# Optimization experiments

Hardware: AMD Instinct MI355X
Metric: run time of the kernel (lower is better)

## Reference

```python
import jax, jax.numpy as jnp
import numpy as np

N = 50000      # nodes
E = 800000     # edges
F_IN = 128     # num_node_features
H = 128        # hidden_channels
C = 10         # num_classes
G = 512        # graphs in batch


def setup_inputs() -> dict:
    key = jax.random.key(0)
    ks = jax.random.split(key, 8)
    x = jax.random.normal(ks[0], (N, F_IN), dtype=jnp.float32)
    edge_index = jax.random.randint(ks[1], (2, E), 0, N, dtype=jnp.int64)
    batch = jnp.sort(jax.random.randint(ks[2], (N,), 0, G, dtype=jnp.int64))
    s = 1.0 / np.sqrt(F_IN)
    W1 = jax.random.normal(ks[3], (F_IN, H), dtype=jnp.float32) * s
    b1 = jnp.zeros((H,), dtype=jnp.float32)
    W2 = jax.random.normal(ks[4], (H, H), dtype=jnp.float32) * s
    b2 = jnp.zeros((H,), dtype=jnp.float32)
    Wl = jax.random.normal(ks[5], (H, C), dtype=jnp.float32) * s
    bl = jnp.zeros((C,), dtype=jnp.float32)
    return {"x": x, "edge_index": edge_index, "batch": batch,
            "W1": W1, "b1": b1, "W2": W2, "b2": b2, "Wl": Wl, "bl": bl}


def _gcn_conv(h, src, dst, deg_inv_sqrt, W, b):
    # PyG GCNConv: x @ W, then symmetric-normalized scatter-add with self-loops.
    h = h @ W                                   # [N, H]
    norm = deg_inv_sqrt[src] * deg_inv_sqrt[dst]  # [E]
    msg = h[src] * norm[:, None]                # gather + scale, [E, H]
    out = jax.ops.segment_sum(msg, dst, num_segments=N)
    # self-loop contribution (deg already includes +1):
    out = out + h * (deg_inv_sqrt * deg_inv_sqrt)[:, None]
    return out + b


def reference(x, edge_index, batch, W1, b1, W2, b2, Wl, bl):
    src, dst = edge_index[0], edge_index[1]
    # degree on destination nodes, +1 for self-loops (PyG default)
    deg = jax.ops.segment_sum(jnp.ones((E,), x.dtype), dst, num_segments=N) + 1.0
    deg_inv_sqrt = jax.lax.rsqrt(deg)

    h = jax.nn.relu(_gcn_conv(x, src, dst, deg_inv_sqrt, W1, b1))
    h = jax.nn.relu(_gcn_conv(h, src, dst, deg_inv_sqrt, W2, b2))

    # global mean pool over graphs
    sums = jax.ops.segment_sum(h, batch, num_segments=G)          # [G, H]
    counts = jax.ops.segment_sum(jnp.ones((N,), h.dtype), batch, num_segments=G)
    pooled = sums / jnp.clip(counts, 1.0)[:, None]
    # dropout p=0.5 is identity in eval mode
    return pooled @ Wl + bl
```

## Files before the change

### kernel.cpp

```cpp
#include <hip/hip_runtime.h>
#include <hip/hip_bf16.h>
#include <hip/hip_fp16.h>

typedef unsigned short ushort_t;
typedef unsigned int uint32;
typedef __attribute__((ext_vector_type(8))) _Float16 half8;
typedef __attribute__((ext_vector_type(4))) float floatx4;

#define KMAX 64
#define BSHIFT 6
#define BCAP2 1280
#define MAXBUK 800

__device__ __forceinline__ uint32 pack2h(float a, float b) {
    return (uint32)__half_as_ushort(__float2half(a)) |
           ((uint32)__half_as_ushort(__float2half(b)) << 16);
}
__device__ __forceinline__ float2 unpack2h(uint32 q) {
    __half2 hh = *reinterpret_cast<__half2*>(&q);
    return __half22float2(hh);
}

__global__ __launch_bounds__(256) void bin_k(const int* __restrict__ ei,
                                             int* __restrict__ bcur,
                                             uint32* __restrict__ binned,
                                             int E, int nbuk) {
    __shared__ int hist[MAXBUK], lbase[MAXBUK];
    int tid = threadIdx.x;
    for (int i = tid; i < nbuk; i += 256) hist[i] = 0;
    __syncthreads();
    int base = blockIdx.x * 4096;
    uint32 ed[16];
    int bk[16];
    #pragma unroll
    for (int i = 0; i < 16; ++i) {
        int e = base + i * 256 + tid;
        if (e < E) {
            int s = ei[e], d = ei[E + e];
            ed[i] = (uint32)s | ((uint32)d << 16);
            bk[i] = d >> BSHIFT;
            atomicAdd(&hist[bk[i]], 1);
        } else bk[i] = -1;
    }
    __syncthreads();
    for (int i = tid; i < nbuk; i += 256) lbase[i] = atomicAdd(&bcur[i], hist[i]);
    __syncthreads();
    for (int i = tid; i < nbuk; i += 256) hist[i] = 0;
    __syncthreads();
    #pragma unroll
    for (int i = 0; i < 16; ++i) {
        if (bk[i] >= 0) {
            int p = atomicAdd(&hist[bk[i]], 1);
            int idx = lbase[bk[i]] + p;
            if (idx < BCAP2) binned[(size_t)bk[i] * BCAP2 + idx] = ed[i];
        }
    }
}

__global__ __launch_bounds__(256) void fill4_k(const uint32* __restrict__ binned,
                                               const int* __restrict__ bcur,
                                               int* __restrict__ cnt,
                                               ushort_t* __restrict__ slot, int N) {
    __shared__ ushort_t ls[64 * KMAX];
    __shared__ int lc[64];
    int b = blockIdx.x;
    int tid = threadIdx.x;
    if (tid < 64) lc[tid] = 0;
    __syncthreads();
    int ne = bcur[b];
    if (ne > BCAP2) ne = BCAP2;
    const uint32* src = binned + (size_t)b * BCAP2;
    int nbase = b << BSHIFT;
    for (int i = tid; i < ne; i += 256) {
        uint32 ed = src[i];
        int s = (int)(ed & 0xFFFFu);
        int d = (int)(ed >> 16) - nbase;
        int p = atomicAdd(&lc[d], 1);
        if (p < KMAX) ls[(d << 6) + p] = (ushort_t)s;
    }
    __syncthreads();
    int nn = N - nbase;
    if (nn > 64) nn = 64;
    if (tid < 64 && tid < nn) cnt[nbase + tid] = lc[tid];
    uint4* gs = (uint4*)(slot + ((size_t)nbase << 6));
    const uint4* lsv = (const uint4*)ls;
    int totalv = nn * 8;
    for (int i = tid; i < totalv; i += 256) gs[i] = lsv[i];
}

__global__ __launch_bounds__(256) void gemm_k(const void* __restrict__ Av, int mode,
                                              const float* __restrict__ W,
                                              uint32* __restrict__ t2, int N,
                                              const int* __restrict__ cnt,
                                              const int* __restrict__ batch,
                                              int* __restrict__ gstart, int G,
                                              int do_bounds) {
    int tid = threadIdx.x;
    if (do_bounds) {
        int i = blockIdx.x * 256 + tid;
        if (i <= G) {
            int lo = 0, hi = N;
            while (lo < hi) {
                int mid = (lo + hi) >> 1;
                if (batch[mid] < i) lo = mid + 1; else hi = mid;
            }
            gstart[i] = lo;
        }
    }

    __shared__ ushort_t Wh[128][136];
    for (int i = tid; i < 128 * 128; i += 256) {
        int k = i >> 7, c = i & 127;
        Wh[c][k] = __half_as_ushort(__float2half(W[i]));
    }
    __syncthreads();

    int wave = tid >> 6, lane = tid & 63;
    int row0 = blockIdx.x * 64 + wave * 16;
    int m = lane & 15;
    int arow = row0 + m;
    int koff = (lane >> 4) * 8;
    bool valid = arow < N;

    floatx4 acc[8];
    #pragma unroll
    for (int nt = 0; nt < 8; ++nt) acc[nt] = (floatx4){0.f, 0.f, 0.f, 0.f};

    for (int kk = 0; kk < 4; ++kk) {
        int k = kk * 32 + koff;
        union { uint32 u[4]; half8 h; } av;
        av.u[0] = av.u[1] = av.u[2] = av.u[3] = 0;
        if (valid) {
            if (mode == 0) {
                const float* p = (const float*)Av + (size_t)arow * 128 + k;
                floatx4 f0 = *(const floatx4*)p;
                floatx4 f1 = *(const floatx4*)(p + 4);
                av.u[0] = pack2h(f0[0], f0[1]);
                av.u[1] = pack2h(f0[2], f0[3]);
                av.u[2] = pack2h(f1[0], f1[1]);
                av.u[3] = pack2h(f1[2], f1[3]);
            } else {
                const uint32* hp = (const uint32*)Av + (size_t)arow * 64 + (k & 63);
                uint4 w0 = *(const uint4*)hp;
                uint4 w1 = *(const uint4*)(hp + 4);
                uint32 ws[8] = {w0.x, w0.y, w0.z, w0.w, w1.x, w1.y, w1.z, w1.w};
                if (k >= 64) {
                    #pragma unroll
                    for (int j = 0; j < 4; ++j)
                        av.u[j] = (ws[2 * j] >> 16) | (ws[2 * j + 1] & 0xFFFF0000u);
                } else {
                    #pragma unroll
                    for (int j = 0; j < 4; ++j)
                        av.u[j] = (ws[2 * j] & 0xFFFFu) | (ws[2 * j + 1] << 16);
                }
            }
        }
        half8 af = av.h;
        #pragma unroll
        for (int nt = 0; nt < 8; ++nt) {
            int col = nt * 16 + m;
            half8 bf = *(const half8*)(&Wh[col][k]);
            acc[nt] = __builtin_amdgcn_mfma_f32_16x16x32_f16(af, bf, acc[nt], 0, 0, 0);
        }
    }

    int r0 = (lane >> 4) * 4;
    float dsc[4];
    #pragma unroll
    for (int r = 0; r < 4; ++r) {
        int row = row0 + r0 + r;
        dsc[r] = (row < N) ? rsqrtf((float)cnt[row] + 1.0f) : 0.f;
    }
    #pragma unroll
    for (int nt = 0; nt < 4; ++nt) {
        int c = nt * 16 + m;
        #pragma unroll
        for (int r = 0; r < 4; ++r) {
            int row = row0 + r0 + r;
            if (row < N)
                t2[(size_t)row * 64 + c] =
                    pack2h(acc[nt][r] * dsc[r], acc[nt + 4][r] * dsc[r]);
        }
    }
}

__global__ __launch_bounds__(256) void agg_k(const uint32* __restrict__ t2,
                                             const int* __restrict__ cnt,
                                             const ushort_t* __restrict__ slot,
                                             const float* __restrict__ bias,
                                             uint32* __restrict__ outp, int N) {
    int wave = threadIdx.x >> 6, lane = threadIdx.x & 63;
    int n = blockIdx.x * 4 + wave;
    if (n >= N) return;
    int deg = cnt[n];
    float d = rsqrtf((float)deg + 1.0f);
    if (deg > KMAX) deg = KMAX;
    float2 self = unpack2h(t2[(size_t)n * 64 + lane]);
    float acc0 = self.x;
    float acc1 = self.y;
    const ushort_t* sl = slot + (size_t)n * KMAX;
    int i = 0;
    for (; i + 16 <= deg; i += 16) {
        uint4 qa = *(const uint4*)(sl + i);
        uint4 qb = *(const uint4*)(sl + i + 8);
        uint32 sw[8] = {qa.x, qa.y, qa.z, qa.w, qb.x, qb.y, qb.z, qb.w};
        int s[16];
        #pragma unroll
        for (int u = 0; u < 8; ++u) {
            s[2 * u] = (int)(sw[u] & 0xFFFFu);
            s[2 * u + 1] = (int)(sw[u] >> 16);
        }
        float2 f[16];
        #pragma unroll
        for (int u = 0; u < 16; ++u)
            f[u] = unpack2h(t2[(size_t)s[u] * 64 + lane]);
        #pragma unroll
        for (int u = 0; u < 16; ++u) {
            acc0 += f[u].x;
            acc1 += f[u].y;
        }
    }
    for (; i + 4 <= deg; i += 4) {
        uint2 qa = *(const uint2*)(sl + i);
        int s[4] = {(int)(qa.x & 0xFFFFu), (int)(qa.x >> 16),
                    (int)(qa.y & 0xFFFFu), (int)(qa.y >> 16)};
        float2 f[4];
        #pragma unroll
        for (int u = 0; u < 4; ++u)
            f[u] = unpack2h(t2[(size_t)s[u] * 64 + lane]);
        #pragma unroll
        for (int u = 0; u < 4; ++u) {
            acc0 += f[u].x;
            acc1 += f[u].y;
        }
    }
    for (; i < deg; ++i) {
        float2 f = unpack2h(t2[(size_t)sl[i] * 64 + lane]);
        acc0 += f.x;
        acc1 += f.y;
    }
    acc0 = fmaxf(acc0 * d + bias[lane], 0.f);
    acc1 = fmaxf(acc1 * d + bias[lane + 64], 0.f);
    outp[(size_t)n * 64 + lane] = pack2h(acc0, acc1);
}

__global__ __launch_bounds__(256) void pool2_k(const uint32* __restrict__ h2,
                                               const int* __restrict__ gstart,
                                               const float* __restrict__ Wl,
                                               const float* __restrict__ bl,
                                               float* __restrict__ out, int C) {
    __shared__ float s0[256];
    __shared__ float s1[256];
    __shared__ float m[128];
    int g = blockIdx.x;
    int s = gstart[g], e = gstart[g + 1];
    int w = threadIdx.x & 63;
    int sub = threadIdx.x >> 6;
    float a0 = 0.f, a1 = 0.f;
    for (int n = s + sub; n < e; n += 4) {
        float2 f = unpack2h(h2[(size_t)n * 64 + w]);
        a0 += f.x;
        a1 += f.y;
    }
    s0[threadIdx.x] = a0;
    s1[threadIdx.x] = a1;
    __syncthreads();
    if (threadIdx.x < 64) {
        float inv = 1.f / fmaxf((float)(e - s), 1.f);
        m[w]      = (s0[w] + s0[w + 64] + s0[w + 128] + s0[w + 192]) * inv;
        m[w + 64] = (s1[w] + s1[w + 64] + s1[w + 128] + s1[w + 192]) * inv;
    }
    __syncthreads();
    if (threadIdx.x < C) {
        float sum = bl[threadIdx.x];
        #pragma unroll 4
        for (int jj = 0; jj < 128; ++jj)
            sum += m[jj] * Wl[jj * C + threadIdx.x];
        out[g * C + threadIdx.x] = sum;
    }
}

extern "C" void kernel_launch(void* const* d_in, const int* in_sizes, int n_in,
                              void* d_out, int out_size, void* d_ws, size_t ws_size,
                              hipStream_t stream) {
    const float* x   = (const float*)d_in[0];
    const int* ei    = (const int*)d_in[1];
    const int* batch = (const int*)d_in[2];
    const float* W1  = (const float*)d_in[3];
    const float* b1  = (const float*)d_in[4];
    const float* W2  = (const float*)d_in[5];
    const float* b2  = (const float*)d_in[6];
    const float* Wl  = (const float*)d_in[7];
    const float* bl  = (const float*)d_in[8];
    float* out = (float*)d_out;

    int N = in_sizes[2];
    int E = in_sizes[1] / 2;
    int C = in_sizes[8];
    int G = out_size / C;
    int nbuk = (N + 63) >> BSHIFT;

    char* w = (char*)d_ws;
    auto alloc = [&](size_t bytes) -> void* {
        void* p = (void*)w;
        w += (bytes + 255) & ~(size_t)255;
        return p;
    };
    int* bcur       = (int*)alloc((size_t)nbuk * 4);
    int* cnt        = (int*)alloc((size_t)N * 4);
    int* gstart     = (int*)alloc((size_t)(G + 1) * 4);
    ushort_t* slot  = (ushort_t*)alloc((size_t)nbuk * 64 * KMAX * 2);
    uint32* binned  = (uint32*)alloc((size_t)nbuk * BCAP2 * 4);
    uint32* t2      = (uint32*)alloc((size_t)N * 64 * 4);
    uint32* h1      = (uint32*)alloc((size_t)N * 64 * 4);
    uint32* h2      = (uint32*)alloc((size_t)N * 64 * 4);

    hipMemsetAsync(bcur, 0, (size_t)nbuk * 4, stream);

    int GB = (N + 63) / 64;
    int AB = (N + 3) / 4;
    int BB = (E + 4095) / 4096;

    bin_k<<<BB, 256, 0, stream>>>(ei, bcur, binned, E, nbuk);
    fill4_k<<<nbuk, 256, 0, stream>>>(binned, bcur, cnt, slot, N);
    gemm_k<<<GB, 256, 0, stream>>>((const void*)x, 0, W1, t2, N,
                                   cnt, batch, gstart, G, 1);
    agg_k<<<AB, 256, 0, stream>>>(t2, cnt, slot, b1, h1, N);
    gemm_k<<<GB, 256, 0, stream>>>((const void*)h1, 2, W2, t2, N,
                                   cnt, batch, gstart, G, 0);
    agg_k<<<AB, 256, 0, stream>>>(t2, cnt, slot, b2, h2, N);
    pool2_k<<<G, 256, 0, stream>>>(h2, gstart, Wl, bl, out, C);
}
```

Measured before the change: 218.3 us.

## Run first GEMM alongside edge binning in one launch, defer degree scaling

Merges the edge-binning kernel and the first-layer GEMM into a single launch in which blocks are split by index: the first BB blocks bin edges and the remaining blocks compute x@W1 plus the graph-boundary search. Because the degree counts are not ready at that point, the GEMM writes unscaled fp16 results and fill4_k later rescales each row by rsqrt(deg+1) once the per-bucket counts are known. This removes one kernel launch and lets the GEMM overlap the atomic-heavy binning. In exchange it adds an extra read-modify-write pass over t2 and a second fp16 rounding step.

```diff
diff --git a/kernel.cpp b/kernel.cpp
--- a/kernel.cpp
+++ b/kernel.cpp
@@ -21,38 +21,105 @@
     return __half22float2(hh);
 }
 
-__global__ __launch_bounds__(256) void bin_k(const int* __restrict__ ei,
-                                             int* __restrict__ bcur,
-                                             uint32* __restrict__ binned,
-                                             int E, int nbuk) {
-    __shared__ int hist[MAXBUK], lbase[MAXBUK];
+__global__ __launch_bounds__(256) void binmm_k(
+    const int* __restrict__ ei, int* __restrict__ bcur,
+    uint32* __restrict__ binned, int E, int nbuk, int BB,
+    const float* __restrict__ x, const float* __restrict__ W,
+    uint32* __restrict__ t2, int N,
+    const int* __restrict__ batch, int* __restrict__ gstart, int G) {
+    __shared__ __align__(16) char smem[34816];
     int tid = threadIdx.x;
-    for (int i = tid; i < nbuk; i += 256) hist[i] = 0;
-    __syncthreads();
-    int base = blockIdx.x * 4096;
-    uint32 ed[16];
-    int bk[16];
-    #pragma unroll
-    for (int i = 0; i < 16; ++i) {
-        int e = base + i * 256 + tid;
-        if (e < E) {
-            int s = ei[e], d = ei[E + e];
-            ed[i] = (uint32)s | ((uint32)d << 16);
-            bk[i] = d >> BSHIFT;
-            atomicAdd(&hist[bk[i]], 1);
-        } else bk[i] = -1;
-    }
-    __syncthreads();
-    for (int i = tid; i < nbuk; i += 256) lbase[i] = atomicAdd(&bcur[i], hist[i]);
-    __syncthreads();
-    for (int i = tid; i < nbuk; i += 256) hist[i] = 0;
-    __syncthreads();
-    #pragma unroll
-    for (int i = 0; i < 16; ++i) {
-        if (bk[i] >= 0) {
-            int p = atomicAdd(&hist[bk[i]], 1);
-            int idx = lbase[bk[i]] + p;
-            if (idx < BCAP2) binned[(size_t)bk[i] * BCAP2 + idx] = ed[i];
+    if (blockIdx.x < BB) {
+        int* hist = (int*)smem;
+        int* lbase = hist + MAXBUK;
+        for (int i = tid; i < nbuk; i += 256) hist[i] = 0;
+        __syncthreads();
+        int base = blockIdx.x * 4096;
+        uint32 ed[16];
+        int bk[16];
+        #pragma unroll
+        for (int i = 0; i < 16; ++i) {
+            int e = base + i * 256 + tid;
+            if (e < E) {
+                int s = ei[e], d = ei[E + e];
+                ed[i] = (uint32)s | ((uint32)d << 16);
+                bk[i] = d >> BSHIFT;
+                atomicAdd(&hist[bk[i]], 1);
+            } else bk[i] = -1;
+        }
+        __syncthreads();
+        for (int i = tid; i < nbuk; i += 256) lbase[i] = atomicAdd(&bcur[i], hist[i]);
+        __syncthreads();
+        for (int i = tid; i < nbuk; i += 256) hist[i] = 0;
+        __syncthreads();
+        #pragma unroll
+        for (int i = 0; i < 16; ++i) {
+            if (bk[i] >= 0) {
+                int p = atomicAdd(&hist[bk[i]], 1);
+                int idx = lbase[bk[i]] + p;
+                if (idx < BCAP2) binned[(size_t)bk[i] * BCAP2 + idx] = ed[i];
+            }
+        }
+    } else {
+        int bid = blockIdx.x - BB;
+        int i0 = bid * 256 + tid;
+        if (i0 <= G) {
+            int lo = 0, hi = N;
+            while (lo < hi) {
+                int mid = (lo + hi) >> 1;
+                if (batch[mid] < i0) lo = mid + 1; else hi = mid;
+            }
+            gstart[i0] = lo;
+        }
+        ushort_t (*Wh)[136] = (ushort_t(*)[136])smem;
+        for (int i = tid; i < 128 * 128; i += 256) {
+            int k = i >> 7, c = i & 127;
+            Wh[c][k] = __half_as_ushort(__float2half(W[i]));
+        }
+        __syncthreads();
+
+        int wave = tid >> 6, lane = tid & 63;
+        int row0 = bid * 64 + wave * 16;
+        int m = lane & 15;
+        int arow = row0 + m;
+        int koff = (lane >> 4) * 8;
+        bool valid = arow < N;
+
+        floatx4 acc[8];
+        #pragma unroll
+        for (int nt = 0; nt < 8; ++nt) acc[nt] = (floatx4){0.f, 0.f, 0.f, 0.f};
+
+        for (int kk = 0; kk < 4; ++kk) {
+            int k = kk * 32 + koff;
+            union { uint32 u[4]; half8 h; } av;
+            av.u[0] = av.u[1] = av.u[2] = av.u[3] = 0;
+            if (valid) {
+                const float* p = x + (size_t)arow * 128 + k;
+                floatx4 f0 = *(const floatx4*)p;
+                floatx4 f1 = *(const floatx4*)(p + 4);
+                av.u[0] = pack2h(f0[0], f0[1]);
+                av.u[1] = pack2h(f0[2], f0[3]);
+                av.u[2] = pack2h(f1[0], f1[1]);
+                av.u[3] = pack2h(f1[2], f1[3]);
+            }
+            half8 af = av.h;
+            #pragma unroll
+            for (int nt = 0; nt < 8; ++nt) {
+                int col = nt * 16 + m;
+                half8 bf = *(const half8*)(&Wh[col][k]);
+                acc[nt] = __builtin_amdgcn_mfma_f32_16x16x32_f16(af, bf, acc[nt], 0, 0, 0);
+            }
+        }
+        int r0 = (lane >> 4) * 4;
+        #pragma unroll
+        for (int nt = 0; nt < 4; ++nt) {
+            int c = nt * 16 + m;
+            #pragma unroll
+            for (int r = 0; r < 4; ++r) {
+                int row = row0 + r0 + r;
+                if (row < N)
+                    t2[(size_t)row * 64 + c] = pack2h(acc[nt][r], acc[nt + 4][r]);
+            }
         }
     }
 }
@@ -60,9 +127,11 @@
 __global__ __launch_bounds__(256) void fill4_k(const uint32* __restrict__ binned,
                                                const int* __restrict__ bcur,
                                                int* __restrict__ cnt,
-                                               ushort_t* __restrict__ slot, int N) {
+                                               ushort_t* __restrict__ slot,
+                                               uint32* __restrict__ t2, int N) {
     __shared__ ushort_t ls[64 * KMAX];
     __shared__ int lc[64];
+    __shared__ float dsf[64];
     int b = blockIdx.x;
     int tid = threadIdx.x;
     if (tid < 64) lc[tid] = 0;
@@ -81,33 +150,30 @@
     __syncthreads();
     int nn = N - nbase;
     if (nn > 64) nn = 64;
-    if (tid < 64 && tid < nn) cnt[nbase + tid] = lc[tid];
+    if (tid < 64) {
+        if (tid < nn) cnt[nbase + tid] = lc[tid];
+        dsf[tid] = rsqrtf((float)lc[tid] + 1.0f);
+    }
     uint4* gs = (uint4*)(slot + ((size_t)nbase << 6));
     const uint4* lsv = (const uint4*)ls;
     int totalv = nn * 8;
     for (int i = tid; i < totalv; i += 256) gs[i] = lsv[i];
-}
-
-__global__ __launch_bounds__(256) void gemm_k(const void* __restrict__ Av, int mode,
-                                              const float* __restrict__ W,
-                                              uint32* __restrict__ t2, int N,
-                                              const int* __restrict__ cnt,
-                                              const int* __restrict__ batch,
-                                              int* __restrict__ gstart, int G,
-                                              int do_bounds) {
+    __syncthreads();
+    int tot = nn * 64;
+    for (int i = tid; i < tot; i += 256) {
+        int r = i >> 6, c = i & 63;
+        size_t idx = ((size_t)(nbase + r) << 6) + c;
+        float ds = dsf[r];
+        float2 f = unpack2h(t2[idx]);
+        t2[idx] = pack2h(f.x * ds, f.y * ds);
+    }
+}
+
+__global__ __launch_bounds__(256) void gemm2_k(const uint32* __restrict__ Av,
+                                               const float* __restrict__ W,
+                                               uint32* __restrict__ t2, int N,
+                                               const int* __restrict__ cnt) {
     int tid = threadIdx.x;
-    if (do_bounds) {
-        int i = blockIdx.x * 256 + tid;
-        if (i <= G) {
-            int lo = 0, hi = N;
-            while (lo < hi) {
-                int mid = (lo + hi) >> 1;
-                if (batch[mid] < i) lo = mid + 1; else hi = mid;
-            }
-            gstart[i] = lo;
-        }
-    }
-
     __shared__ ushort_t Wh[128][136];
     for (int i = tid; i < 128 * 128; i += 256) {
         int k = i >> 7, c = i & 127;
@@ -131,28 +197,18 @@
         union { uint32 u[4]; half8 h; } av;
         av.u[0] = av.u[1] = av.u[2] = av.u[3] = 0;
         if (valid) {
-            if (mode == 0) {
-                const float* p = (const float*)Av + (size_t)arow * 128 + k;
-                floatx4 f0 = *(const floatx4*)p;
-                floatx4 f1 = *(const floatx4*)(p + 4);
-                av.u[0] = pack2h(f0[0], f0[1]);
-                av.u[1] = pack2h(f0[2], f0[3]);
-                av.u[2] = pack2h(f1[0], f1[1]);
-                av.u[3] = pack2h(f1[2], f1[3]);
+            const uint32* hp = Av + (size_t)arow * 64 + (k & 63);
+            uint4 w0 = *(const uint4*)hp;
+            uint4 w1 = *(const uint4*)(hp + 4);
+            uint32 ws[8] = {w0.x, w0.y, w0.z, w0.w, w1.x, w1.y, w1.z, w1.w};
+            if (k >= 64) {
+                #pragma unroll
+                for (int j = 0; j < 4; ++j)
+                    av.u[j] = (ws[2 * j] >> 16) | (ws[2 * j + 1] & 0xFFFF0000u);
             } else {
-                const uint32* hp = (const uint32*)Av + (size_t)arow * 64 + (k & 63);
-                uint4 w0 = *(const uint4*)hp;
-                uint4 w1 = *(const uint4*)(hp + 4);
-                uint32 ws[8] = {w0.x, w0.y, w0.z, w0.w, w1.x, w1.y, w1.z, w1.w};
-                if (k >= 64) {
-                    #pragma unroll
-                    for (int j = 0; j < 4; ++j)
-                        av.u[j] = (ws[2 * j] >> 16) | (ws[2 * j + 1] & 0xFFFF0000u);
-                } else {
-                    #pragma unroll
-                    for (int j = 0; j < 4; ++j)
-                        av.u[j] = (ws[2 * j] & 0xFFFFu) | (ws[2 * j + 1] << 16);
-                }
+                #pragma unroll
+                for (int j = 0; j < 4; ++j)
+                    av.u[j] = (ws[2 * j] & 0xFFFFu) | (ws[2 * j + 1] << 16);
             }
         }
         half8 af = av.h;
@@ -321,13 +377,11 @@
     int AB = (N + 3) / 4;
     int BB = (E + 4095) / 4096;
 
-    bin_k<<<BB, 256, 0, stream>>>(ei, bcur, binned, E, nbuk);
-    fill4_k<<<nbuk, 256, 0, stream>>>(binned, bcur, cnt, slot, N);
-    gemm_k<<<GB, 256, 0, stream>>>((const void*)x, 0, W1, t2, N,
-                                   cnt, batch, gstart, G, 1);
+    binmm_k<<<BB + GB, 256, 0, stream>>>(ei, bcur, binned, E, nbuk, BB,
+                                         x, W1, t2, N, batch, gstart, G);
+    fill4_k<<<nbuk, 256, 0, stream>>>(binned, bcur, cnt, slot, t2, N);
     agg_k<<<AB, 256, 0, stream>>>(t2, cnt, slot, b1, h1, N);
-    gemm_k<<<GB, 256, 0, stream>>>((const void*)h1, 2, W2, t2, N,
-                                   cnt, batch, gstart, G, 0);
+    gemm2_k<<<GB, 256, 0, stream>>>(h1, W2, t2, N, cnt);
     agg_k<<<AB, 256, 0, stream>>>(t2, cnt, slot, b2, h2, N);
     pool2_k<<<G, 256, 0, stream>>>(h2, gstart, Wl, bl, out, C);
 }
```

After: 209.8 us. 3.9% less time.
